# Kernel optimization log

Measured on AMD Instinct MI355X. Metric: run time of the kernel, lower is better.

The kernel has to match this reference:

```python
import jax, jax.numpy as jnp
import numpy as np

N = 50000
IN_C = 128
OUT_C = 64


def gcn_conv(x, edge_index, W, b):
    # PyG GCNConv: h = X W; add self-loops; symmetric norm D^-1/2 (A+I) D^-1/2; aggregate; + bias
    n = x.shape[0]
    h = x @ W  # [N, out]
    loop = jnp.arange(n, dtype=edge_index.dtype)
    row = jnp.concatenate([edge_index[0], loop])  # source
    col = jnp.concatenate([edge_index[1], loop])  # target
    deg = jax.ops.segment_sum(jnp.ones_like(col, dtype=h.dtype), col, num_segments=n)
    dinv = jnp.where(deg > 0, jax.lax.rsqrt(deg), 0.0)
    norm = dinv[row] * dinv[col]  # [E+N]
    msg = norm[:, None] * h[row]  # gather source features
    out = jax.ops.segment_sum(msg, col, num_segments=n)  # scatter to targets
    return out + b


def layer_norm(x, w, b, eps=1e-5):
    mu = jnp.mean(x, axis=-1, keepdims=True)
    var = jnp.mean((x - mu) ** 2, axis=-1, keepdims=True)
    return (x - mu) * jax.lax.rsqrt(var + eps) * w + b


def setup_inputs() -> dict:
    key = jax.random.key(0)
    ks = jax.random.split(key, 10)
    x = jax.random.normal(ks[0], (N, IN_C), dtype=jnp.float32)
    edge_index = jax.random.randint(ks[1], (2, 800000), 0, N, dtype=jnp.int64)
    s1 = 1.0 / np.sqrt(IN_C)
    s2 = 1.0 / np.sqrt(OUT_C)
    W1 = jax.random.uniform(ks[2], (IN_C, OUT_C), jnp.float32, -s1, s1)
    b1 = jnp.zeros((OUT_C,), jnp.float32)
    ln_w = jnp.ones((OUT_C,), jnp.float32)
    ln_b = jnp.zeros((OUT_C,), jnp.float32)
    W2 = jax.random.uniform(ks[3], (OUT_C, OUT_C), jnp.float32, -s2, s2)
    b2 = jnp.zeros((OUT_C,), jnp.float32)
    W3 = jax.random.uniform(ks[4], (OUT_C, 6), jnp.float32, -s2, s2)
    b3 = jax.random.uniform(ks[5], (6,), jnp.float32, -s2, s2)
    return {"x": x, "edge_index": edge_index, "W1": W1, "b1": b1,
            "ln_w": ln_w, "ln_b": ln_b, "W2": W2, "b2": b2, "W3": W3, "b3": b3}


def reference(x, edge_index, W1, b1, ln_w, ln_b, W2, b2, W3, b3):
    h = gcn_conv(x, edge_index, W1, b1)           # [N, 64]
    h = jax.nn.relu(layer_norm(h, ln_w, ln_b))    # [N, 64]
    out1 = gcn_conv(h, edge_index, W2, b2)        # [N, 64]
    out2 = jax.nn.sigmoid(h @ W3 + b3)            # [N, 6]
    return (out1, out2)
```

## Files before the change

kernel.cpp:

```cpp
#include <hip/hip_runtime.h>
#include <hip/hip_fp16.h>
#include <math.h>


#define ELLW 48

typedef _Float16 half8 __attribute__((ext_vector_type(8)));
typedef float f32x4 __attribute__((ext_vector_type(4)));

__global__ void k_init(int* __restrict__ cnt, int n) {
    int i = blockIdx.x * blockDim.x + threadIdx.x;
    if (i < n) cnt[i] = 0;
}

__global__ __launch_bounds__(256) void k_scatter(
    const int* __restrict__ row, const int* __restrict__ col,
    int* __restrict__ cnt, int* __restrict__ ell, int E, int slice_sz) {
    int slice = blockIdx.x & 7;
    int lo = slice * slice_sz;
    int hi = lo + slice_sz;
    int nchunk = gridDim.x >> 3;
    int stride = nchunk * 256;
    int v0 = (blockIdx.x >> 3) * 256 + threadIdx.x;
    int nv = E >> 2;
    const int4* c4p = (const int4*)col;
    const int4* r4p = (const int4*)row;
    for (int v = v0; v < nv; v += stride) {
        int4 c4 = c4p[v];
        int4 r4 = r4p[v];
        if (c4.x >= lo && c4.x < hi) {
            int rk = atomicAdd(&cnt[c4.x], 1);
            if (rk < ELLW) ell[c4.x * ELLW + rk] = r4.x << 7;
        }
        if (c4.y >= lo && c4.y < hi) {
            int rk = atomicAdd(&cnt[c4.y], 1);
            if (rk < ELLW) ell[c4.y * ELLW + rk] = r4.y << 7;
        }
        if (c4.z >= lo && c4.z < hi) {
            int rk = atomicAdd(&cnt[c4.z], 1);
            if (rk < ELLW) ell[c4.z * ELLW + rk] = r4.z << 7;
        }
        if (c4.w >= lo && c4.w < hi) {
            int rk = atomicAdd(&cnt[c4.w], 1);
            if (rk < ELLW) ell[c4.w * ELLW + rk] = r4.w << 7;
        }
    }
    if ((blockIdx.x >> 3) == 0) {
        for (int e = (nv << 2) + threadIdx.x; e < E; e += 256) {
            int c = col[e];
            if (c >= lo && c < hi) {
                int rk = atomicAdd(&cnt[c], 1);
                if (rk < ELLW) ell[c * ELLW + rk] = row[e] << 7;
            }
        }
    }
}

__global__ void k_dinv(const int* __restrict__ cnt, float* __restrict__ dinv, int n) {
    int i = blockIdx.x * blockDim.x + threadIdx.x;
    if (i < n) dinv[i] = rsqrtf((float)(cnt[i] + 1));
}

__global__ void k_pack(const float* __restrict__ W1, const float* __restrict__ W2,
                       const float* __restrict__ W3, _Float16* __restrict__ W1g,
                       _Float16* __restrict__ Bg) {
    int idx = blockIdx.x * 256 + threadIdx.x;
    if (idx < 8192) {
        int j = idx & 7, L = (idx >> 3) & 63, s = (idx >> 9) & 3, t = idx >> 11;
        int k = s * 32 + (L >> 4) * 8 + j;
        int c = t * 16 + (L & 15);
        W1g[idx] = (_Float16)W1[k * 64 + c];
    } else if (idx < 8192 + 5120) {
        int i2 = idx - 8192;
        int j = i2 & 7, L = (i2 >> 3) & 63, s = (i2 >> 9) & 1, u = i2 >> 10;
        int k = s * 32 + (L >> 4) * 8 + j;
        int c = (L & 15);
        float v;
        if (u < 4) v = W2[k * 64 + u * 16 + c];
        else v = (c < 6) ? W3[k * 6 + c] : 0.f;
        Bg[i2] = (_Float16)v;
    }
}

__global__ __launch_bounds__(256, 4) void k_gemm1(
    const float* __restrict__ x, const _Float16* __restrict__ W1g,
    const float* __restrict__ dinv, uint* __restrict__ hs,
    uint* __restrict__ h2s, int n) {
    int tid = threadIdx.x;
    if (blockIdx.x == 0) {
        if (tid < 32) hs[(size_t)n * 32 + tid] = 0u;
        else if (tid < 64) h2s[(size_t)n * 32 + (tid - 32)] = 0u;
    }
    int lane = tid & 63, wid = tid >> 6;
    int m16 = lane & 15, quad = lane >> 4;
    int node0 = blockIdx.x * 64 + wid * 16;
    int arow = node0 + m16;
    if (arow >= n) arow = n - 1;
    const float* xr = x + (size_t)arow * 128;
    half8 A[4];
#pragma unroll
    for (int s = 0; s < 4; s++) {
        const float4* p = (const float4*)(xr + s * 32 + quad * 8);
        float4 f0 = p[0], f1 = p[1];
        half8 a;
        a[0] = (_Float16)f0.x; a[1] = (_Float16)f0.y;
        a[2] = (_Float16)f0.z; a[3] = (_Float16)f0.w;
        a[4] = (_Float16)f1.x; a[5] = (_Float16)f1.y;
        a[6] = (_Float16)f1.z; a[7] = (_Float16)f1.w;
        A[s] = a;
    }
    float dsc[4];
#pragma unroll
    for (int r = 0; r < 4; r++) {
        int nd = node0 + quad * 4 + r;
        dsc[r] = dinv[nd < n ? nd : n - 1];
    }
    const half8* Wv = (const half8*)W1g;
#pragma unroll
    for (int t = 0; t < 4; t++) {
        f32x4 acc = {0.f, 0.f, 0.f, 0.f};
#pragma unroll
        for (int s = 0; s < 4; s++)
            acc = __builtin_amdgcn_mfma_f32_16x16x32_f16(A[s], Wv[(t * 4 + s) * 64 + lane], acc, 0, 0, 0);
#pragma unroll
        for (int r = 0; r < 4; r++) {
            int nd = node0 + quad * 4 + r;
            float v = acc[r] * dsc[r];
            float vo = __shfl_xor(v, 1, 64);
            if (!(m16 & 1) && nd < n) {
                __half2 pk = __floats2half2_rn(v, vo);
                hs[(size_t)nd * 32 + t * 8 + (m16 >> 1)] = *(uint*)&pk;
            }
        }
    }
}

#define GATHER_BODY(SRC)                                                      \
    int4 o1[4], o2[4];                                                        \
    uint4 u0[4], u1[4];                                                       \
    {                                                                         \
        int4 o0[4];                                                           \
        _Pragma("unroll") for (int p = 0; p < 4; p++) o0[p] = ldidx(p, 0);    \
        _Pragma("unroll") for (int p = 0; p < 4; p++) o1[p] = ldidx(p, 8);    \
        _Pragma("unroll") for (int p = 0; p < 4; p++) {                       \
            u0[p].x = *(const uint*)(SRC + o0[p].x + m4);                     \
            u0[p].y = *(const uint*)(SRC + o0[p].y + m4);                     \
            u0[p].z = *(const uint*)(SRC + o0[p].z + m4);                     \
            u0[p].w = *(const uint*)(SRC + o0[p].w + m4);                     \
        }                                                                     \
    }                                                                         \
    for (int jb = 0; jb < Pmax; jb += 8) {                                    \
        _Pragma("unroll") for (int p = 0; p < 4; p++) o2[p] = ldidx(p, jb + 16); \
        _Pragma("unroll") for (int p = 0; p < 4; p++) {                       \
            u1[p].x = *(const uint*)(SRC + o1[p].x + m4);                     \
            u1[p].y = *(const uint*)(SRC + o1[p].y + m4);                     \
            u1[p].z = *(const uint*)(SRC + o1[p].z + m4);                     \
            u1[p].w = *(const uint*)(SRC + o1[p].w + m4);                     \
        }                                                                     \
        _Pragma("unroll") for (int p = 0; p < 4; p++) {                       \
            float2 f;                                                         \
            f = __half22float2(*(__half2*)&u0[p].x); ax[p] += f.x; ay[p] += f.y; \
            f = __half22float2(*(__half2*)&u0[p].y); ax[p] += f.x; ay[p] += f.y; \
            f = __half22float2(*(__half2*)&u0[p].z); ax[p] += f.x; ay[p] += f.y; \
            f = __half22float2(*(__half2*)&u0[p].w); ax[p] += f.x; ay[p] += f.y; \
        }                                                                     \
        _Pragma("unroll") for (int p = 0; p < 4; p++) { o1[p] = o2[p]; u0[p] = u1[p]; } \
    }

__global__ __launch_bounds__(256, 4) void k_conv1_fused(
    const uint* __restrict__ hs, const int* __restrict__ ell,
    const int* __restrict__ cnt, const float* __restrict__ dinv,
    const float* __restrict__ b1, const float* __restrict__ lnw_g,
    const float* __restrict__ lnb_g, const _Float16* __restrict__ Bg,
    const float* __restrict__ b3, uint* __restrict__ h2s,
    float* __restrict__ out2, int zoff, int n) {
    __shared__ _Float16 Y[4][16 * 72];
    int tid = threadIdx.x;
    int lane = tid & 63, wid = tid >> 6;
    int m = lane & 31, g = lane >> 5;
    int m4 = m * 4;
    {
        float4 z = {0.f, 0.f, 0.f, 0.f};
        float4* yb = (float4*)Y[wid];
        for (int i = lane; i < 144; i += 64) yb[i] = z;
    }
    int base = blockIdx.x * 16;
    int nid[4], st[4], P[4];
    int Pmax = 0;
#pragma unroll
    for (int p = 0; p < 4; p++) {
        int node = base + wid * 4 + p;
        if (node >= n) node = n - 1;
        nid[p] = node;
        st[p] = node * ELLW;
        P[p] = cnt[node];
        Pmax = Pmax > P[p] ? Pmax : P[p];
    }
    Pmax = (Pmax + 7) & ~7;
    auto ldidx = [&](int p, int jb) -> int4 {
        int4 o = *(const int4*)(ell + st[p] + jb + 4 * g);
        int b = jb + 4 * g;
        o.x = (b + 0 < P[p]) ? o.x : zoff;
        o.y = (b + 1 < P[p]) ? o.y : zoff;
        o.z = (b + 2 < P[p]) ? o.z : zoff;
        o.w = (b + 3 < P[p]) ? o.w : zoff;
        return o;
    };
    const char* hsb = (const char*)hs;
    float ax[4], ay[4];
#pragma unroll
    for (int p = 0; p < 4; p++) {
        int sa = (g == 0) ? (nid[p] << 7) : zoff;
        uint us = *(const uint*)(hsb + sa + m4);
        float2 f = __half22float2(*(__half2*)&us);
        ax[p] = f.x; ay[p] = f.y;
    }
    GATHER_BODY(hsb)

    float2 b1v = ((const float2*)b1)[m];
    float2 lw = ((const float2*)lnw_g)[m];
    float2 lb = ((const float2*)lnb_g)[m];
    float dcs[4];
#pragma unroll
    for (int p = 0; p < 4; p++) {
        float axp = ax[p] + __shfl_xor(ax[p], 32, 64);
        float ayp = ay[p] + __shfl_xor(ay[p], 32, 64);
        float dc = dinv[nid[p]];
        dcs[p] = dc;
        float va = fmaf(dc, axp, b1v.x);
        float vb = fmaf(dc, ayp, b1v.y);
        float s = va + vb;
#pragma unroll
        for (int off = 16; off > 0; off >>= 1) s += __shfl_xor(s, off, 64);
        float mu = s * (1.f / 64.f);
        float da = va - mu, db = vb - mu;
        float q = da * da + db * db;
#pragma unroll
        for (int off = 16; off > 0; off >>= 1) q += __shfl_xor(q, off, 64);
        float rstd = rsqrtf(q * (1.f / 64.f) + 1e-5f);
        float yA = fmaxf(fmaf(da * rstd, lw.x, lb.x), 0.f);
        float yB = fmaxf(fmaf(db * rstd, lw.y, lb.y), 0.f);
        if (g == 0) {
            __half2 pk = __floats2half2_rn(yA, yB);
            *(__half2*)&Y[wid][p * 72 + 2 * m] = pk;
        }
    }
    int m16 = lane & 15, quad = lane >> 4;
    half8 a0 = *(const half8*)&Y[wid][m16 * 72 + quad * 8];
    half8 a1 = *(const half8*)&Y[wid][m16 * 72 + 32 + quad * 8];
    const half8* Bv = (const half8*)Bg;
    _Float16* h2h = (_Float16*)h2s;
#pragma unroll
    for (int t = 0; t < 4; t++) {
        f32x4 acc = {0.f, 0.f, 0.f, 0.f};
        acc = __builtin_amdgcn_mfma_f32_16x16x32_f16(a0, Bv[(t * 2 + 0) * 64 + lane], acc, 0, 0, 0);
        acc = __builtin_amdgcn_mfma_f32_16x16x32_f16(a1, Bv[(t * 2 + 1) * 64 + lane], acc, 0, 0, 0);
#pragma unroll
        for (int r = 0; r < 4; r++) {
            int nodep = base + wid * 4 + r;
            if (quad == 0 && nodep < n)
                h2h[(size_t)nodep * 64 + t * 16 + m16] = (_Float16)(acc[r] * dcs[r]);
        }
    }
    {
        f32x4 acc = {0.f, 0.f, 0.f, 0.f};
        acc = __builtin_amdgcn_mfma_f32_16x16x32_f16(a0, Bv[8 * 64 + lane], acc, 0, 0, 0);
        acc = __builtin_amdgcn_mfma_f32_16x16x32_f16(a1, Bv[9 * 64 + lane], acc, 0, 0, 0);
        float bb = b3[m16 < 6 ? m16 : 0];
#pragma unroll
        for (int r = 0; r < 4; r++) {
            int nodep = base + wid * 4 + r;
            if (quad == 0 && m16 < 6 && nodep < n)
                out2[(size_t)nodep * 6 + m16] = 1.f / (1.f + __expf(-(acc[r] + bb)));
        }
    }
}

__global__ __launch_bounds__(256, 4) void k_conv2(
    const uint* __restrict__ h2s, const int* __restrict__ ell,
    const int* __restrict__ cnt, const float* __restrict__ dinv,
    const float* __restrict__ b2, float* __restrict__ out1, int zoff, int n) {
    int tid = threadIdx.x;
    int lane = tid & 63, wid = tid >> 6;
    int m = lane & 31, g = lane >> 5;
    int m4 = m * 4;
    int base = blockIdx.x * 16;
    int nid[4], st[4], P[4];
    int Pmax = 0;
#pragma unroll
    for (int p = 0; p < 4; p++) {
        int node = base + wid * 4 + p;
        if (node >= n) node = n - 1;
        nid[p] = node;
        st[p] = node * ELLW;
        P[p] = cnt[node];
        Pmax = Pmax > P[p] ? Pmax : P[p];
    }
    Pmax = (Pmax + 7) & ~7;
    auto ldidx = [&](int p, int jb) -> int4 {
        int4 o = *(const int4*)(ell + st[p] + jb + 4 * g);
        int b = jb + 4 * g;
        o.x = (b + 0 < P[p]) ? o.x : zoff;
        o.y = (b + 1 < P[p]) ? o.y : zoff;
        o.z = (b + 2 < P[p]) ? o.z : zoff;
        o.w = (b + 3 < P[p]) ? o.w : zoff;
        return o;
    };
    const char* hsb = (const char*)h2s;
    float ax[4], ay[4];
#pragma unroll
    for (int p = 0; p < 4; p++) {
        int sa = (g == 0) ? (nid[p] << 7) : zoff;
        uint us = *(const uint*)(hsb + sa + m4);
        float2 f = __half22float2(*(__half2*)&us);
        ax[p] = f.x; ay[p] = f.y;
    }
    GATHER_BODY(hsb)

    float2 b2v = ((const float2*)b2)[m];
#pragma unroll
    for (int p = 0; p < 4; p++) {
        float axp = ax[p] + __shfl_xor(ax[p], 32, 64);
        float ayp = ay[p] + __shfl_xor(ay[p], 32, 64);
        int node = base + wid * 4 + p;
        if (g == 0 && node < n) {
            float dc = dinv[nid[p]];
            float2 r;
            r.x = fmaf(dc, axp, b2v.x);
            r.y = fmaf(dc, ayp, b2v.y);
            ((float2*)out1)[(size_t)node * 32 + m] = r;
        }
    }
}

extern "C" void kernel_launch(void* const* d_in, const int* in_sizes, int n_in,
                              void* d_out, int out_size, void* d_ws, size_t ws_size,
                              hipStream_t stream) {
    const float* x   = (const float*)d_in[0];
    const int*   ei  = (const int*)d_in[1];
    const float* W1  = (const float*)d_in[2];
    const float* b1  = (const float*)d_in[3];
    const float* lnw = (const float*)d_in[4];
    const float* lnb = (const float*)d_in[5];
    const float* W2  = (const float*)d_in[6];
    const float* b2  = (const float*)d_in[7];
    const float* W3  = (const float*)d_in[8];
    const float* b3  = (const float*)d_in[9];

    int n = in_sizes[0] / 128;
    int E = in_sizes[1] / 2;
    const int* row = ei;
    const int* col = ei + E;

    char* ws = (char*)d_ws;
    size_t off = 0;
    auto carve = [&](size_t bytes) -> char* {
        char* p = ws + off;
        off = (off + bytes + 255) & ~(size_t)255;
        return p;
    };
    int*   cnt  = (int*)carve(4 * (size_t)n);
    float* dinv = (float*)carve(4 * (size_t)n);
    int*   ell  = (int*)carve(4 * ((size_t)n * ELLW + 256));
    uint*  hs   = (uint*)carve(128 * ((size_t)n + 1));
    uint*  h2s  = (uint*)carve(128 * ((size_t)n + 1));
    _Float16* W1g = (_Float16*)carve(2 * 8192);
    _Float16* Bg  = (_Float16*)carve(2 * 5120);

    float* out1 = (float*)d_out;
    float* out2 = out1 + (size_t)n * 64;
    int zero_off = n << 7;
    int slice_sz = (n + 7) / 8;

    k_pack<<<52, 256, 0, stream>>>(W1, W2, W3, W1g, Bg);
    k_init<<<(n + 255) / 256, 256, 0, stream>>>(cnt, n);
    k_scatter<<<8 * 256, 256, 0, stream>>>(row, col, cnt, ell, E, slice_sz);
    k_dinv<<<(n + 255) / 256, 256, 0, stream>>>(cnt, dinv, n);
    k_gemm1<<<(n + 63) / 64, 256, 0, stream>>>(x, W1g, dinv, hs, h2s, n);
    k_conv1_fused<<<(n + 15) / 16, 256, 0, stream>>>(hs, ell, cnt, dinv,
                                                     b1, lnw, lnb, Bg, b3,
                                                     h2s, out2, zero_off, n);
    k_conv2<<<(n + 15) / 16, 256, 0, stream>>>(h2s, ell, cnt, dinv, b2,
                                               out1, zero_off, n);
}
```

Before: 202.5 us.

## Merge setup kernels, compute dinv inline, and widen gather to 8-byte loads

Combines the weight-pack and count-init kernels into one launch and drops the dinv kernel and buffer, recomputing rsqrt(cnt+1) inline wherever it is needed. The gather loops in both conv kernels now have each lane load 4 halves (8 bytes) per neighbour, with four lane groups covering 16 column slots instead of two groups of 32. This halves the number of index loads per lane but needs two extra shuffle stages to reduce the partial sums. The aim is to cut launch overhead and improve gather memory efficiency.

```diff
diff --git a/kernel.cpp b/kernel.cpp
--- a/kernel.cpp
+++ b/kernel.cpp
@@ -8,9 +8,30 @@
 typedef _Float16 half8 __attribute__((ext_vector_type(8)));
 typedef float f32x4 __attribute__((ext_vector_type(4)));
 
-__global__ void k_init(int* __restrict__ cnt, int n) {
-    int i = blockIdx.x * blockDim.x + threadIdx.x;
-    if (i < n) cnt[i] = 0;
+__global__ void k_setup(const float* __restrict__ W1, const float* __restrict__ W2,
+                        const float* __restrict__ W3, _Float16* __restrict__ W1g,
+                        _Float16* __restrict__ Bg, int* __restrict__ cnt, int n) {
+    if (blockIdx.x >= 52) {
+        int i = (blockIdx.x - 52) * 256 + threadIdx.x;
+        if (i < n) cnt[i] = 0;
+        return;
+    }
+    int idx = blockIdx.x * 256 + threadIdx.x;
+    if (idx < 8192) {
+        int j = idx & 7, L = (idx >> 3) & 63, s = (idx >> 9) & 3, t = idx >> 11;
+        int k = s * 32 + (L >> 4) * 8 + j;
+        int c = t * 16 + (L & 15);
+        W1g[idx] = (_Float16)W1[k * 64 + c];
+    } else if (idx < 8192 + 5120) {
+        int i2 = idx - 8192;
+        int j = i2 & 7, L = (i2 >> 3) & 63, s = (i2 >> 9) & 1, u = i2 >> 10;
+        int k = s * 32 + (L >> 4) * 8 + j;
+        int c = (L & 15);
+        float v;
+        if (u < 4) v = W2[k * 64 + u * 16 + c];
+        else v = (c < 6) ? W3[k * 6 + c] : 0.f;
+        Bg[i2] = (_Float16)v;
+    }
 }
 
 __global__ __launch_bounds__(256) void k_scatter(
@@ -56,35 +77,9 @@
     }
 }
 
-__global__ void k_dinv(const int* __restrict__ cnt, float* __restrict__ dinv, int n) {
-    int i = blockIdx.x * blockDim.x + threadIdx.x;
-    if (i < n) dinv[i] = rsqrtf((float)(cnt[i] + 1));
-}
-
-__global__ void k_pack(const float* __restrict__ W1, const float* __restrict__ W2,
-                       const float* __restrict__ W3, _Float16* __restrict__ W1g,
-                       _Float16* __restrict__ Bg) {
-    int idx = blockIdx.x * 256 + threadIdx.x;
-    if (idx < 8192) {
-        int j = idx & 7, L = (idx >> 3) & 63, s = (idx >> 9) & 3, t = idx >> 11;
-        int k = s * 32 + (L >> 4) * 8 + j;
-        int c = t * 16 + (L & 15);
-        W1g[idx] = (_Float16)W1[k * 64 + c];
-    } else if (idx < 8192 + 5120) {
-        int i2 = idx - 8192;
-        int j = i2 & 7, L = (i2 >> 3) & 63, s = (i2 >> 9) & 1, u = i2 >> 10;
-        int k = s * 32 + (L >> 4) * 8 + j;
-        int c = (L & 15);
-        float v;
-        if (u < 4) v = W2[k * 64 + u * 16 + c];
-        else v = (c < 6) ? W3[k * 6 + c] : 0.f;
-        Bg[i2] = (_Float16)v;
-    }
-}
-
 __global__ __launch_bounds__(256, 4) void k_gemm1(
     const float* __restrict__ x, const _Float16* __restrict__ W1g,
-    const float* __restrict__ dinv, uint* __restrict__ hs,
+    const int* __restrict__ cnt, uint* __restrict__ hs,
     uint* __restrict__ h2s, int n) {
     int tid = threadIdx.x;
     if (blockIdx.x == 0) {
@@ -113,7 +108,7 @@
 #pragma unroll
     for (int r = 0; r < 4; r++) {
         int nd = node0 + quad * 4 + r;
-        dsc[r] = dinv[nd < n ? nd : n - 1];
+        dsc[r] = rsqrtf((float)(cnt[nd < n ? nd : n - 1] + 1));
     }
     const half8* Wv = (const half8*)W1g;
 #pragma unroll
@@ -135,114 +130,121 @@
     }
 }
 
-#define GATHER_BODY(SRC)                                                      \
-    int4 o1[4], o2[4];                                                        \
+#define GATHER_BODY8(SRC)                                                     \
+    int2 o1[4], o2[4];                                                        \
     uint4 u0[4], u1[4];                                                       \
     {                                                                         \
-        int4 o0[4];                                                           \
-        _Pragma("unroll") for (int p = 0; p < 4; p++) o0[p] = ldidx(p, 0);    \
-        _Pragma("unroll") for (int p = 0; p < 4; p++) o1[p] = ldidx(p, 8);    \
+        int2 o0[4];                                                           \
+        _Pragma("unroll") for (int p = 0; p < 4; p++) o0[p] = ldidx2(p, 0);   \
+        _Pragma("unroll") for (int p = 0; p < 4; p++) o1[p] = ldidx2(p, 8);   \
         _Pragma("unroll") for (int p = 0; p < 4; p++) {                       \
-            u0[p].x = *(const uint*)(SRC + o0[p].x + m4);                     \
-            u0[p].y = *(const uint*)(SRC + o0[p].y + m4);                     \
-            u0[p].z = *(const uint*)(SRC + o0[p].z + m4);                     \
-            u0[p].w = *(const uint*)(SRC + o0[p].w + m4);                     \
+            uint2 t0 = *(const uint2*)(SRC + o0[p].x + m8);                   \
+            uint2 t1 = *(const uint2*)(SRC + o0[p].y + m8);                   \
+            u0[p].x = t0.x; u0[p].y = t0.y; u0[p].z = t1.x; u0[p].w = t1.y;   \
         }                                                                     \
     }                                                                         \
     for (int jb = 0; jb < Pmax; jb += 8) {                                    \
-        _Pragma("unroll") for (int p = 0; p < 4; p++) o2[p] = ldidx(p, jb + 16); \
+        _Pragma("unroll") for (int p = 0; p < 4; p++) o2[p] = ldidx2(p, jb + 16); \
         _Pragma("unroll") for (int p = 0; p < 4; p++) {                       \
-            u1[p].x = *(const uint*)(SRC + o1[p].x + m4);                     \
-            u1[p].y = *(const uint*)(SRC + o1[p].y + m4);                     \
-            u1[p].z = *(const uint*)(SRC + o1[p].z + m4);                     \
-            u1[p].w = *(const uint*)(SRC + o1[p].w + m4);                     \
+            uint2 t0 = *(const uint2*)(SRC + o1[p].x + m8);                   \
+            uint2 t1 = *(const uint2*)(SRC + o1[p].y + m8);                   \
+            u1[p].x = t0.x; u1[p].y = t0.y; u1[p].z = t1.x; u1[p].w = t1.y;   \
         }                                                                     \
         _Pragma("unroll") for (int p = 0; p < 4; p++) {                       \
             float2 f;                                                         \
-            f = __half22float2(*(__half2*)&u0[p].x); ax[p] += f.x; ay[p] += f.y; \
-            f = __half22float2(*(__half2*)&u0[p].y); ax[p] += f.x; ay[p] += f.y; \
-            f = __half22float2(*(__half2*)&u0[p].z); ax[p] += f.x; ay[p] += f.y; \
-            f = __half22float2(*(__half2*)&u0[p].w); ax[p] += f.x; ay[p] += f.y; \
+            f = __half22float2(*(__half2*)&u0[p].x); acc[p][0] += f.x; acc[p][1] += f.y; \
+            f = __half22float2(*(__half2*)&u0[p].y); acc[p][2] += f.x; acc[p][3] += f.y; \
+            f = __half22float2(*(__half2*)&u0[p].z); acc[p][0] += f.x; acc[p][1] += f.y; \
+            f = __half22float2(*(__half2*)&u0[p].w); acc[p][2] += f.x; acc[p][3] += f.y; \
         }                                                                     \
         _Pragma("unroll") for (int p = 0; p < 4; p++) { o1[p] = o2[p]; u0[p] = u1[p]; } \
     }
 
+#define GATHER_PROLOG(SRC_T)                                                  \
+    int nid[4], st[4], P[4];                                                  \
+    int Pmax = 0;                                                             \
+    _Pragma("unroll") for (int p = 0; p < 4; p++) {                           \
+        int node = base + wid * 4 + p;                                        \
+        if (node >= n) node = n - 1;                                          \
+        nid[p] = node;                                                        \
+        st[p] = node * ELLW;                                                  \
+        P[p] = cnt[node];                                                     \
+        Pmax = Pmax > P[p] ? Pmax : P[p];                                     \
+    }                                                                         \
+    Pmax = (Pmax + 7) & ~7;                                                   \
+    auto ldidx2 = [&](int p, int jb) -> int2 {                                \
+        int2 o = *(const int2*)(ell + st[p] + jb + 2 * g);                    \
+        int b = jb + 2 * g;                                                   \
+        o.x = (b + 0 < P[p]) ? o.x : zoff;                                    \
+        o.y = (b + 1 < P[p]) ? o.y : zoff;                                    \
+        return o;                                                             \
+    };                                                                        \
+    const char* hsb = (const char*)(SRC_T);                                   \
+    f32x4 acc[4];                                                             \
+    _Pragma("unroll") for (int p = 0; p < 4; p++) {                           \
+        int sa = (g == 0) ? (nid[p] << 7) : zoff;                             \
+        uint2 us = *(const uint2*)(hsb + sa + m8);                            \
+        float2 f0 = __half22float2(*(__half2*)&us.x);                         \
+        float2 f1 = __half22float2(*(__half2*)&us.y);                         \
+        acc[p][0] = f0.x; acc[p][1] = f0.y; acc[p][2] = f1.x; acc[p][3] = f1.y; \
+    }
+
 __global__ __launch_bounds__(256, 4) void k_conv1_fused(
     const uint* __restrict__ hs, const int* __restrict__ ell,
-    const int* __restrict__ cnt, const float* __restrict__ dinv,
-    const float* __restrict__ b1, const float* __restrict__ lnw_g,
-    const float* __restrict__ lnb_g, const _Float16* __restrict__ Bg,
-    const float* __restrict__ b3, uint* __restrict__ h2s,
-    float* __restrict__ out2, int zoff, int n) {
+    const int* __restrict__ cnt, const float* __restrict__ b1,
+    const float* __restrict__ lnw_g, const float* __restrict__ lnb_g,
+    const _Float16* __restrict__ Bg, const float* __restrict__ b3,
+    uint* __restrict__ h2s, float* __restrict__ out2, int zoff, int n) {
     __shared__ _Float16 Y[4][16 * 72];
     int tid = threadIdx.x;
     int lane = tid & 63, wid = tid >> 6;
-    int m = lane & 31, g = lane >> 5;
-    int m4 = m * 4;
+    int m16l = lane & 15, g = lane >> 4;
+    int m8 = m16l * 8;
     {
         float4 z = {0.f, 0.f, 0.f, 0.f};
         float4* yb = (float4*)Y[wid];
         for (int i = lane; i < 144; i += 64) yb[i] = z;
     }
     int base = blockIdx.x * 16;
-    int nid[4], st[4], P[4];
-    int Pmax = 0;
+    GATHER_PROLOG(hs)
+    GATHER_BODY8(hsb)
+
+    float4 b1v = ((const float4*)b1)[m16l];
+    float4 lw = ((const float4*)lnw_g)[m16l];
+    float4 lb = ((const float4*)lnb_g)[m16l];
+    float dcs[4];
 #pragma unroll
     for (int p = 0; p < 4; p++) {
-        int node = base + wid * 4 + p;
-        if (node >= n) node = n - 1;
-        nid[p] = node;
-        st[p] = node * ELLW;
-        P[p] = cnt[node];
-        Pmax = Pmax > P[p] ? Pmax : P[p];
-    }
-    Pmax = (Pmax + 7) & ~7;
-    auto ldidx = [&](int p, int jb) -> int4 {
-        int4 o = *(const int4*)(ell + st[p] + jb + 4 * g);
-        int b = jb + 4 * g;
-        o.x = (b + 0 < P[p]) ? o.x : zoff;
-        o.y = (b + 1 < P[p]) ? o.y : zoff;
-        o.z = (b + 2 < P[p]) ? o.z : zoff;
-        o.w = (b + 3 < P[p]) ? o.w : zoff;
-        return o;
-    };
-    const char* hsb = (const char*)hs;
-    float ax[4], ay[4];
-#pragma unroll
-    for (int p = 0; p < 4; p++) {
-        int sa = (g == 0) ? (nid[p] << 7) : zoff;
-        uint us = *(const uint*)(hsb + sa + m4);
-        float2 f = __half22float2(*(__half2*)&us);
-        ax[p] = f.x; ay[p] = f.y;
-    }
-    GATHER_BODY(hsb)
-
-    float2 b1v = ((const float2*)b1)[m];
-    float2 lw = ((const float2*)lnw_g)[m];
-    float2 lb = ((const float2*)lnb_g)[m];
-    float dcs[4];
-#pragma unroll
-    for (int p = 0; p < 4; p++) {
-        float axp = ax[p] + __shfl_xor(ax[p], 32, 64);
-        float ayp = ay[p] + __shfl_xor(ay[p], 32, 64);
-        float dc = dinv[nid[p]];
+        float s0 = acc[p][0], s1 = acc[p][1], s2 = acc[p][2], s3 = acc[p][3];
+        s0 += __shfl_xor(s0, 16, 64); s0 += __shfl_xor(s0, 32, 64);
+        s1 += __shfl_xor(s1, 16, 64); s1 += __shfl_xor(s1, 32, 64);
+        s2 += __shfl_xor(s2, 16, 64); s2 += __shfl_xor(s2, 32, 64);
+        s3 += __shfl_xor(s3, 16, 64); s3 += __shfl_xor(s3, 32, 64);
+        float dc = rsqrtf((float)(P[p] + 1));
         dcs[p] = dc;
-        float va = fmaf(dc, axp, b1v.x);
-        float vb = fmaf(dc, ayp, b1v.y);
-        float s = va + vb;
-#pragma unroll
-        for (int off = 16; off > 0; off >>= 1) s += __shfl_xor(s, off, 64);
+        float v0 = fmaf(dc, s0, b1v.x);
+        float v1 = fmaf(dc, s1, b1v.y);
+        float v2 = fmaf(dc, s2, b1v.z);
+        float v3 = fmaf(dc, s3, b1v.w);
+        float s = v0 + v1 + v2 + v3;
+#pragma unroll
+        for (int off = 8; off > 0; off >>= 1) s += __shfl_xor(s, off, 64);
         float mu = s * (1.f / 64.f);
-        float da = va - mu, db = vb - mu;
-        float q = da * da + db * db;
-#pragma unroll
-        for (int off = 16; off > 0; off >>= 1) q += __shfl_xor(q, off, 64);
+        float d0 = v0 - mu, d1 = v1 - mu, d2 = v2 - mu, d3 = v3 - mu;
+        float q = d0 * d0 + d1 * d1 + d2 * d2 + d3 * d3;
+#pragma unroll
+        for (int off = 8; off > 0; off >>= 1) q += __shfl_xor(q, off, 64);
         float rstd = rsqrtf(q * (1.f / 64.f) + 1e-5f);
-        float yA = fmaxf(fmaf(da * rstd, lw.x, lb.x), 0.f);
-        float yB = fmaxf(fmaf(db * rstd, lw.y, lb.y), 0.f);
+        float y0 = fmaxf(fmaf(d0 * rstd, lw.x, lb.x), 0.f);
+        float y1 = fmaxf(fmaf(d1 * rstd, lw.y, lb.y), 0.f);
+        float y2 = fmaxf(fmaf(d2 * rstd, lw.z, lb.z), 0.f);
+        float y3 = fmaxf(fmaf(d3 * rstd, lw.w, lb.w), 0.f);
         if (g == 0) {
-            __half2 pk = __floats2half2_rn(yA, yB);
-            *(__half2*)&Y[wid][p * 72 + 2 * m] = pk;
+            __half2 pk0 = __floats2half2_rn(y0, y1);
+            __half2 pk1 = __floats2half2_rn(y2, y3);
+            uint2 pk;
+            pk.x = *(uint*)&pk0; pk.y = *(uint*)&pk1;
+            *(uint2*)&Y[wid][p * 72 + 4 * m16l] = pk;
         }
     }
     int m16 = lane & 15, quad = lane >> 4;
@@ -252,83 +254,59 @@
     _Float16* h2h = (_Float16*)h2s;
 #pragma unroll
     for (int t = 0; t < 4; t++) {
-        f32x4 acc = {0.f, 0.f, 0.f, 0.f};
-        acc = __builtin_amdgcn_mfma_f32_16x16x32_f16(a0, Bv[(t * 2 + 0) * 64 + lane], acc, 0, 0, 0);
-        acc = __builtin_amdgcn_mfma_f32_16x16x32_f16(a1, Bv[(t * 2 + 1) * 64 + lane], acc, 0, 0, 0);
+        f32x4 acc2 = {0.f, 0.f, 0.f, 0.f};
+        acc2 = __builtin_amdgcn_mfma_f32_16x16x32_f16(a0, Bv[(t * 2 + 0) * 64 + lane], acc2, 0, 0, 0);
+        acc2 = __builtin_amdgcn_mfma_f32_16x16x32_f16(a1, Bv[(t * 2 + 1) * 64 + lane], acc2, 0, 0, 0);
 #pragma unroll
         for (int r = 0; r < 4; r++) {
             int nodep = base + wid * 4 + r;
             if (quad == 0 && nodep < n)
-                h2h[(size_t)nodep * 64 + t * 16 + m16] = (_Float16)(acc[r] * dcs[r]);
+                h2h[(size_t)nodep * 64 + t * 16 + m16] = (_Float16)(acc2[r] * dcs[r]);
         }
     }
     {
-        f32x4 acc = {0.f, 0.f, 0.f, 0.f};
-        acc = __builtin_amdgcn_mfma_f32_16x16x32_f16(a0, Bv[8 * 64 + lane], acc, 0, 0, 0);
-        acc = __builtin_amdgcn_mfma_f32_16x16x32_f16(a1, Bv[9 * 64 + lane], acc, 0, 0, 0);
+        f32x4 acc2 = {0.f, 0.f, 0.f, 0.f};
+        acc2 = __builtin_amdgcn_mfma_f32_16x16x32_f16(a0, Bv[8 * 64 + lane], acc2, 0, 0, 0);
+        acc2 = __builtin_amdgcn_mfma_f32_16x16x32_f16(a1, Bv[9 * 64 + lane], acc2, 0, 0, 0);
         float bb = b3[m16 < 6 ? m16 : 0];
 #pragma unroll
         for (int r = 0; r < 4; r++) {
             int nodep = base + wid * 4 + r;
             if (quad == 0 && m16 < 6 && nodep < n)
-                out2[(size_t)nodep * 6 + m16] = 1.f / (1.f + __expf(-(acc[r] + bb)));
+                out2[(size_t)nodep * 6 + m16] = 1.f / (1.f + __expf(-(acc2[r] + bb)));
         }
     }
 }
 
 __global__ __launch_bounds__(256, 4) void k_conv2(
     const uint* __restrict__ h2s, const int* __restrict__ ell,
-    const int* __restrict__ cnt, const float* __restrict__ dinv,
-    const float* __restrict__ b2, float* __restrict__ out1, int zoff, int n) {
+    const int* __restrict__ cnt, const float* __restrict__ b2,
+    float* __restrict__ out1, int zoff, int n) {
     int tid = threadIdx.x;
     int lane = tid & 63, wid = tid >> 6;
-    int m = lane & 31, g = lane >> 5;
-    int m4 = m * 4;
+    int m16l = lane & 15, g = lane >> 4;
+    int m8 = m16l * 8;
     int base = blockIdx.x * 16;
-    int nid[4], st[4], P[4];
-    int Pmax = 0;
+    GATHER_PROLOG(h2s)
+    GATHER_BODY8(hsb)
+
+    float4 b2v = ((const float4*)b2)[m16l];
 #pragma unroll
     for (int p = 0; p < 4; p++) {
-        int node = base + wid * 4 + p;
-        if (node >= n) node = n - 1;
-        nid[p] = node;
-        st[p] = node * ELLW;
-        P[p] = cnt[node];
-        Pmax = Pmax > P[p] ? Pmax : P[p];
-    }
-    Pmax = (Pmax + 7) & ~7;
-    auto ldidx = [&](int p, int jb) -> int4 {
-        int4 o = *(const int4*)(ell + st[p] + jb + 4 * g);
-        int b = jb + 4 * g;
-        o.x = (b + 0 < P[p]) ? o.x : zoff;
-        o.y = (b + 1 < P[p]) ? o.y : zoff;
-        o.z = (b + 2 < P[p]) ? o.z : zoff;
-        o.w = (b + 3 < P[p]) ? o.w : zoff;
-        return o;
-    };
-    const char* hsb = (const char*)h2s;
-    float ax[4], ay[4];
-#pragma unroll
-    for (int p = 0; p < 4; p++) {
-        int sa = (g == 0) ? (nid[p] << 7) : zoff;
-        uint us = *(const uint*)(hsb + sa + m4);
-        float2 f = __half22float2(*(__half2*)&us);
-        ax[p] = f.x; ay[p] = f.y;
-    }
-    GATHER_BODY(hsb)
-
-    float2 b2v = ((const float2*)b2)[m];
-#pragma unroll
-    for (int p = 0; p < 4; p++) {
-        float axp = ax[p] + __shfl_xor(ax[p], 32, 64);
-        float ayp = ay[p] + __shfl_xor(ay[p], 32, 64);
+        float s0 = acc[p][0], s1 = acc[p][1], s2 = acc[p][2], s3 = acc[p][3];
+        s0 += __shfl_xor(s0, 16, 64); s0 += __shfl_xor(s0, 32, 64);
+        s1 += __shfl_xor(s1, 16, 64); s1 += __shfl_xor(s1, 32, 64);
+        s2 += __shfl_xor(s2, 16, 64); s2 += __shfl_xor(s2, 32, 64);
+        s3 += __shfl_xor(s3, 16, 64); s3 += __shfl_xor(s3, 32, 64);
         int node = base + wid * 4 + p;
         if (g == 0 && node < n) {
-            float dc = dinv[nid[p]];
-            float2 r;
-            r.x = fmaf(dc, axp, b2v.x);
-            r.y = fmaf(dc, ayp, b2v.y);
-            ((float2*)out1)[(size_t)node * 32 + m] = r;
+            float dc = rsqrtf((float)(P[p] + 1));
+            float4 r;
+            r.x = fmaf(dc, s0, b2v.x);
+            r.y = fmaf(dc, s1, b2v.y);
+            r.z = fmaf(dc, s2, b2v.z);
+            r.w = fmaf(dc, s3, b2v.w);
+            ((float4*)out1)[(size_t)node * 16 + m16l] = r;
         }
     }
 }
@@ -360,7 +338,6 @@
         return p;
     };
     int*   cnt  = (int*)carve(4 * (size_t)n);
-    float* dinv = (float*)carve(4 * (size_t)n);
     int*   ell  = (int*)carve(4 * ((size_t)n * ELLW + 256));
     uint*  hs   = (uint*)carve(128 * ((size_t)n + 1));
     uint*  h2s  = (uint*)carve(128 * ((size_t)n + 1));
@@ -372,14 +349,12 @@
     int zero_off = n << 7;
     int slice_sz = (n + 7) / 8;
 
-    k_pack<<<52, 256, 0, stream>>>(W1, W2, W3, W1g, Bg);
-    k_init<<<(n + 255) / 256, 256, 0, stream>>>(cnt, n);
+    k_setup<<<52 + (n + 255) / 256, 256, 0, stream>>>(W1, W2, W3, W1g, Bg, cnt, n);
     k_scatter<<<8 * 256, 256, 0, stream>>>(row, col, cnt, ell, E, slice_sz);
-    k_dinv<<<(n + 255) / 256, 256, 0, stream>>>(cnt, dinv, n);
-    k_gemm1<<<(n + 63) / 64, 256, 0, stream>>>(x, W1g, dinv, hs, h2s, n);
-    k_conv1_fused<<<(n + 15) / 16, 256, 0, stream>>>(hs, ell, cnt, dinv,
+    k_gemm1<<<(n + 63) / 64, 256, 0, stream>>>(x, W1g, cnt, hs, h2s, n);
+    k_conv1_fused<<<(n + 15) / 16, 256, 0, stream>>>(hs, ell, cnt,
                                                      b1, lnw, lnb, Bg, b3,
                                                      h2s, out2, zero_off, n);
-    k_conv2<<<(n + 15) / 16, 256, 0, stream>>>(h2s, ell, cnt, dinv, b2,
+    k_conv2<<<(n + 15) / 16, 256, 0, stream>>>(h2s, ell, cnt, b2,
                                                out1, zero_off, n);
 }
```

New measurement: 187.6 us. 1.08x faster.
